# Performance work log

Hardware: AMD Instinct MI355X
Metric: run time of the kernel (lower is better)

## Reference

```python
import jax, jax.numpy as jnp
import numpy as np

WIN = 8   # window size
NH = 6    # num heads
DIM = 192
PDIM = 256
S = 32    # D=H=W spatial extent


def window_partition(x, w):
    # x: (B, D, H, W, C) -> (nW, w**3, C)
    B, D, H, Wd, C = x.shape
    x = x.reshape(B, D // w, w, H // w, w, Wd // w, w, C)
    x = x.transpose(0, 1, 3, 5, 2, 4, 6, 7)
    return x.reshape(-1, w * w * w, C)


def window_reverse(win, w, B, D, H, Wd):
    C = win.shape[-1]
    x = win.reshape(B, D // w, H // w, Wd // w, w, w, w, C)
    x = x.transpose(0, 1, 4, 2, 5, 3, 6, 7)
    return x.reshape(B, D, H, Wd, C)


def layernorm(x, g, b, eps=1e-5):
    m = x.mean(-1, keepdims=True)
    v = ((x - m) ** 2).mean(-1, keepdims=True)
    return (x - m) / jnp.sqrt(v + eps) * g + b


def setup_inputs() -> dict:
    key = jax.random.key(0)
    ks = jax.random.split(key, 8)
    return {
        "x": jax.random.normal(ks[0], (1, DIM, S, S, S), jnp.float32),
        "prev_x": jax.random.normal(ks[1], (1, PDIM, S, S, S), jnp.float32),
        "fc1_w": jax.random.normal(ks[2], (PDIM, PDIM), jnp.float32) * 0.02,
        "fc1_b": jnp.zeros((PDIM,), jnp.float32),
        "fc2_w": jax.random.normal(ks[3], (DIM, PDIM), jnp.float32) * 0.02,
        "fc2_b": jnp.zeros((DIM,), jnp.float32),
        "q_w": jax.random.normal(ks[4], (DIM, DIM), jnp.float32) * 0.02,
        "q_b": jnp.zeros((DIM,), jnp.float32),
        "kv_w": jax.random.normal(ks[5], (2 * DIM, DIM), jnp.float32) * 0.02,
        "v_b": jnp.zeros((DIM,), jnp.float32),
        "proj_w": jax.random.normal(ks[6], (DIM, DIM), jnp.float32) * 0.02,
        "proj_b": jnp.zeros((DIM,), jnp.float32),
        "logit_scale": jnp.log(10.0) * jnp.ones((NH, 1, 1), jnp.float32),
        "ln_g": jnp.ones((DIM,), jnp.float32),
        "ln_b": jnp.zeros((DIM,), jnp.float32),
    }


def reference(x, prev_x, fc1_w, fc1_b, fc2_w, fc2_b, q_w, q_b, kv_w, v_b,
              proj_w, proj_b, logit_scale, ln_g, ln_b):
    B, C, D, H, Wd = x.shape
    xc = x.transpose(0, 2, 3, 4, 1)       # (B, D, H, W, C)
    pc = prev_x.transpose(0, 2, 3, 4, 1)   # (B, D, H, W, prev_dim)
    # mlp_match: Linear -> GELU(exact) -> Linear
    pc = jax.nn.gelu(pc @ fc1_w.T + fc1_b, approximate=False) @ fc2_w.T + fc2_b
    xw = window_partition(xc, WIN)         # (nW, N, C)
    pw = window_partition(pc, WIN)         # (nW, N, C)
    nW, N, _ = xw.shape
    hd = C // NH
    # q from x1, kv from x2 (k has no bias, v does)
    q = (xw @ q_w.T + q_b).reshape(nW, N, NH, hd).transpose(0, 2, 1, 3)
    kv_bias = jnp.concatenate([jnp.zeros_like(v_b), v_b])
    kv = (pw @ kv_w.T + kv_bias).reshape(nW, N, 2, NH, hd).transpose(2, 0, 3, 1, 4)
    k_, v_ = kv[0], kv[1]                  # (nW, H, N, hd)
    # cosine attention with clamped learned logit scale
    qn = q / jnp.maximum(jnp.linalg.norm(q, axis=-1, keepdims=True), 1e-12)
    kn = k_ / jnp.maximum(jnp.linalg.norm(k_, axis=-1, keepdims=True), 1e-12)
    scale = jnp.exp(jnp.minimum(logit_scale, jnp.log(1.0 / 0.01)))  # (H,1,1)
    attn = jnp.einsum('whnd,whmd->whnm', qn, kn) * scale
    attn = jax.nn.softmax(attn, axis=-1)
    out = jnp.einsum('whnm,whmd->whnd', attn, v_).transpose(0, 2, 1, 3).reshape(nW, N, C)
    out = out @ proj_w.T + proj_b
    xw = xw + layernorm(out, ln_g, ln_b)   # residual + cross_norm
    xr = window_reverse(xw, WIN, B, D, H, Wd)
    return xr.transpose(0, 4, 1, 2, 3)     # back to (B, C, D, H, W)
```

## Files before the change

kernel.cpp:

```cpp
#include <hip/hip_runtime.h>
#include <stdint.h>

typedef unsigned short u16;
typedef unsigned int u32;
typedef short short8 __attribute__((ext_vector_type(8)));
typedef float f32x4 __attribute__((ext_vector_type(4)));
typedef u32 u32x4 __attribute__((ext_vector_type(4)));

#define T_TOT 32768

__device__ __forceinline__ u16 f2bf(float f) {
  u32 u = __float_as_uint(f);
  return (u16)((u + 0x7fffu + ((u >> 16) & 1u)) >> 16);
}
__device__ __forceinline__ float bf2f(u16 h) {
  return __uint_as_float(((u32)h) << 16);
}
__device__ __forceinline__ u32 pk2(float a, float b) {
  return (u32)f2bf(a) | ((u32)f2bf(b) << 16);
}
__device__ __forceinline__ u32 cvtpk(float a, float b) {
  u32 r;
  asm("v_cvt_pk_bf16_f32 %0, %1, %2" : "=v"(r) : "v"(a), "v"(b));
  return r;
}
__device__ __forceinline__ void unp8(uint4 d, float* v) {
  u32 dd[4] = {d.x, d.y, d.z, d.w};
#pragma unroll
  for (int q2 = 0; q2 < 4; ++q2) {
    v[q2 * 2]     = bf2f((u16)(dd[q2] & 0xffffu));
    v[q2 * 2 + 1] = bf2f((u16)(dd[q2] >> 16));
  }
}

__device__ __forceinline__ void gld_lds16(const void* g, void* l) {
  __builtin_amdgcn_global_load_lds(
      (const __attribute__((address_space(1))) u32*)g,
      (__attribute__((address_space(3))) u32*)l, 16, 0, 0);
}

__device__ __forceinline__ void plswap(u32& a, u32& b) {
#if __has_builtin(__builtin_amdgcn_permlane32_swap) && \
    __has_builtin(__builtin_amdgcn_permlane16_swap)
  typedef u32 u32x2v __attribute__((ext_vector_type(2)));
  u32x2v r = __builtin_amdgcn_permlane32_swap(a, b, false, false);
  u32x2v w = __builtin_amdgcn_permlane16_swap(r[0], r[1], false, false);
  a = w[0]; b = w[1];
#else
  asm volatile(
      "s_nop 2\n\t"
      "v_permlane32_swap_b32 %0, %1\n\t"
      "s_nop 2\n\t"
      "v_permlane16_swap_b32 %0, %1\n\t"
      "s_nop 2"
      : "+v"(a), "+v"(b));
#endif
}

__global__ __launch_bounds__(256) void k_wconv(
    const float* __restrict__ fc1, const float* __restrict__ fc2,
    const float* __restrict__ qw, const float* __restrict__ kvw,
    const float* __restrict__ pw, u16* __restrict__ out) {
  int idx = blockIdx.x * 256 + threadIdx.x;
  const float* src; int K; int rel; u16* dst;
  if (idx < 8192)       { src = fc1; K = 256; rel = idx;         dst = out; }
  else if (idx < 14336) { src = fc2; K = 256; rel = idx - 8192;  dst = out + 65536; }
  else if (idx < 18944) { src = qw;  K = 192; rel = idx - 14336; dst = out + 114688; }
  else if (idx < 28160) { src = kvw; K = 192; rel = idx - 18944; dst = out + 151552; }
  else                  { src = pw;  K = 192; rel = idx - 28160; dst = out + 225280; }
  int nch = K >> 3;
  int m = rel / nch, ch = rel % nch;
  const float* sp = src + (size_t)m * K + ch * 8;
  int pos = (ch & ~7) | ((ch ^ m) & 7);
  u16* dp = dst + (size_t)m * K + pos * 8;
  ushort4 u0, u1;
  u0.x = f2bf(sp[0]); u0.y = f2bf(sp[1]); u0.z = f2bf(sp[2]); u0.w = f2bf(sp[3]);
  u1.x = f2bf(sp[4]); u1.y = f2bf(sp[5]); u1.z = f2bf(sp[6]); u1.w = f2bf(sp[7]);
  *(ushort4*)(dp) = u0;
  *(ushort4*)(dp + 4) = u1;
}

template<int C>
__global__ __launch_bounds__(256) void k_transpose(const float* __restrict__ src,
                                                   u16* __restrict__ dst) {
  __shared__ u16 sT[64][72];
  int c0 = blockIdx.x * 64, t0 = blockIdx.y * 64;
  int tid = threadIdx.x;
  for (int i = tid; i < 1024; i += 256) {
    int row = i >> 4;
    int tb  = (i & 15) * 4;
    const float* sp = src + (size_t)(c0 + row) * T_TOT + t0 + tb;
    float4 v = *(const float4*)sp;
    ushort4 u;
    u.x = f2bf(v.x); u.y = f2bf(v.y); u.z = f2bf(v.z); u.w = f2bf(v.w);
    *(ushort4*)(&sT[row][tb]) = u;
  }
  __syncthreads();
  int tl = tid & 63;
  int jb = tid >> 6;
  for (int p = 0; p < 2; ++p) {
    int j = jb + 4 * p;
    int t = t0 + tl;
    u16 e[8];
#pragma unroll
    for (int e8 = 0; e8 < 8; ++e8) e[e8] = sT[j * 8 + e8][tl];
    int pos = (c0 >> 3) + (j ^ (t & 7));
    uint4 o;
    o.x = (u32)e[0] | ((u32)e[1] << 16);
    o.y = (u32)e[2] | ((u32)e[3] << 16);
    o.z = (u32)e[4] | ((u32)e[5] << 16);
    o.w = (u32)e[6] | ((u32)e[7] << 16);
    *(uint4*)(dst + (size_t)t * C + pos * 8) = o;
  }
}

enum { EPI_FC1 = 0, EPI_FC2 = 1, EPI_Q = 2, EPI_KV = 3 };

template<int M, int K, int EPI>
__global__ __launch_bounds__(256) void k_gemm(const u16* __restrict__ W,
    const u16* __restrict__ B, const float* __restrict__ bias,
    u16* __restrict__ out, u16* __restrict__ out2) {
  __shared__ u16 lW[64 * 64];
  __shared__ u16 lB[128 * 64];
  int tid = threadIdx.x;
  int lane = tid & 63, wid = tid >> 6;
  int g = lane >> 4, c = lane & 15;
  int wm = wid >> 1, wt = wid & 1;
  int t0 = blockIdx.x * 128, m0 = blockIdx.y * 64;
  f32x4 acc[2][4];
#pragma unroll
  for (int i = 0; i < 2; ++i)
#pragma unroll
    for (int j = 0; j < 4; ++j) acc[i][j] = f32x4{0.f, 0.f, 0.f, 0.f};

  for (int s = 0; s < K / 64; ++s) {
    __syncthreads();
#pragma unroll
    for (int i0 = 0; i0 < 512; i0 += 256) {
      int i = i0 + tid;
      int r = i >> 3, ch = i & 7;
      gld_lds16(W + (size_t)(m0 + r) * K + s * 64 + ch * 8,
                lW + (size_t)(i & ~63) * 8);
    }
#pragma unroll
    for (int i0 = 0; i0 < 1024; i0 += 256) {
      int i = i0 + tid;
      int r = i >> 3, ch = i & 7;
      gld_lds16(B + (size_t)(t0 + r) * K + s * 64 + ch * 8,
                lB + (size_t)(i & ~63) * 8);
    }
    __syncthreads();
#pragma unroll
    for (int kc = 0; kc < 2; ++kc) {
      short8 af[2], bfr[4];
#pragma unroll
      for (int mt = 0; mt < 2; ++mt) {
        int r = wm * 32 + mt * 16 + c;
        af[mt] = *(const short8*)(lW + r * 64 + (((kc * 4 + g) ^ (r & 7)) << 3));
      }
#pragma unroll
      for (int tt = 0; tt < 4; ++tt) {
        int r = wt * 64 + tt * 16 + c;
        bfr[tt] = *(const short8*)(lB + r * 64 + (((kc * 4 + g) ^ (r & 7)) << 3));
      }
#pragma unroll
      for (int mt = 0; mt < 2; ++mt)
#pragma unroll
        for (int tt = 0; tt < 4; ++tt)
          acc[mt][tt] = __builtin_amdgcn_mfma_f32_16x16x32_bf16(
              af[mt], bfr[tt], acc[mt][tt], 0, 0, 0);
    }
  }

#pragma unroll
  for (int mt = 0; mt < 2; ++mt) {
    int m_base = m0 + wm * 32 + mt * 16 + 4 * g;
    float br[4];
    if constexpr (EPI == EPI_KV) {
      if (m_base < 192) { br[0] = br[1] = br[2] = br[3] = 0.f; }
      else {
        float4 b4 = *(const float4*)(bias + (m_base - 192));
        br[0] = b4.x; br[1] = b4.y; br[2] = b4.z; br[3] = b4.w;
      }
    } else {
      float4 b4 = *(const float4*)(bias + m_base);
      br[0] = b4.x; br[1] = b4.y; br[2] = b4.z; br[3] = b4.w;
    }
#pragma unroll
    for (int tt = 0; tt < 4; ++tt) {
      int t = t0 + wt * 64 + tt * 16 + c;
      float v[4];
#pragma unroll
      for (int r = 0; r < 4; ++r) v[r] = acc[mt][tt][r] + br[r];
      if constexpr (EPI == EPI_FC1) {
#pragma unroll
        for (int r = 0; r < 4; ++r)
          v[r] = 0.5f * v[r] * (1.0f + erff(v[r] * 0.70710678118654752f));
      }
      if constexpr (EPI == EPI_FC1 || EPI == EPI_FC2) {
        ushort4 u;
        u.x = f2bf(v[0]); u.y = f2bf(v[1]); u.z = f2bf(v[2]); u.w = f2bf(v[3]);
        int pos = (m_base >> 3) ^ (t & 7);
        *(ushort4*)(out + (size_t)t * M + (pos << 3) + (m_base & 7)) = u;
      } else {
        int z = t >> 10, y = (t >> 5) & 31, xx = t & 31;
        int win = ((z >> 3) << 4) + ((y >> 3) << 2) + (xx >> 3);
        int n = ((z & 7) << 6) + ((y & 7) << 3) + (xx & 7);
        if (EPI == EPI_Q || m_base < 192) {
          int head = m_base >> 5, dim = m_base & 31;
          ushort4 u;
          u.x = f2bf(v[0]); u.y = f2bf(v[1]); u.z = f2bf(v[2]); u.w = f2bf(v[3]);
          *(ushort4*)(out + ((size_t)(win * 6 + head) * 512 + n) * 32 + dim) = u;
        } else {
          int vb = m_base - 192;
          int head = vb >> 5, dimb = vb & 31;
#pragma unroll
          for (int r = 0; r < 4; ++r) {
            int dimr = dimb + r;
            out2[((size_t)(win * 6 + head) * 32 + dimr) * 512 +
                 (((n >> 3) ^ (dimr & 7)) << 3) + (n & 7)] = f2bf(v[r]);
          }
        }
      }
    }
  }
}

__global__ __launch_bounds__(256) void k_attn(const u16* __restrict__ Qw,
    const u16* __restrict__ Kw, const u16* __restrict__ Vw,
    const float* __restrict__ ls, u16* __restrict__ Amat) {
  __shared__ u16 Kn[512 * 36];
  int tid = threadIdx.x, lane = tid & 63, wid = tid >> 6;
  int g = lane >> 4, c = lane & 15;
  int zq = blockIdx.x / 6, head = blockIdx.x % 6, win = blockIdx.y;
  const u16* Kg = Kw + (size_t)(win * 6 + head) * 16384;
  const u16* Vg = Vw + (size_t)(win * 6 + head) * 16384;
  const u16* Qg = Qw + (size_t)(win * 6 + head) * 16384;
  for (int i = tid; i < 2048; i += 256) {
    int r = i >> 2, ch = i & 3;
    *(uint4*)(Kn + r * 36 + ch * 8) = *(const uint4*)(Kg + (size_t)i * 8);
  }
  __syncthreads();

#pragma unroll
  for (int rep = 0; rep < 2; ++rep) {
    u16* kp = Kn + (rep * 256 + tid) * 36;
    float v[32];
    unp8(*(const uint4*)(kp), v);
    unp8(*(const uint4*)(kp + 8), v + 8);
    unp8(*(const uint4*)(kp + 16), v + 16);
    unp8(*(const uint4*)(kp + 24), v + 24);
    float ss = 0.f;
#pragma unroll
    for (int e = 0; e < 32; ++e) ss += v[e] * v[e];
    float rn = 1.0f / fmaxf(sqrtf(ss), 1e-12f);
#pragma unroll
    for (int i2 = 0; i2 < 4; ++i2) {
      uint4 d;
      d.x = pk2(v[i2 * 8 + 0] * rn, v[i2 * 8 + 1] * rn);
      d.y = pk2(v[i2 * 8 + 2] * rn, v[i2 * 8 + 3] * rn);
      d.z = pk2(v[i2 * 8 + 4] * rn, v[i2 * 8 + 5] * rn);
      d.w = pk2(v[i2 * 8 + 6] * rn, v[i2 * 8 + 7] * rn);
      *(uint4*)(kp + i2 * 8) = d;
    }
  }
  __syncthreads();

  float sl2e = __expf(fminf(ls[head], 4.6051701859880914f)) * 1.4426950408889634f;
  int wz = win >> 4, wy = (win >> 2) & 3, wx = win & 3;
  u32x4 onepk;
  onepk[0] = 0x3F803F80u; onepk[1] = 0x3F803F80u;
  onepk[2] = 0x3F803F80u; onepk[3] = 0x3F803F80u;
  short8 ONES = __builtin_bit_cast(short8, onepk);

  for (int qp = 0; qp < 2; ++qp) {
    int q0A = zq * 256 + wid * 64 + qp * 32;
    int q0B = q0A + 16;
    uint4 qrA = *(const uint4*)(Qg + (size_t)(q0A + c) * 32 + g * 8);
    uint4 qrB = *(const uint4*)(Qg + (size_t)(q0B + c) * 32 + g * 8);
    float qvA[8], qvB[8];
    unp8(qrA, qvA);
    unp8(qrB, qvB);
    float ssA = 0.f, ssB = 0.f;
#pragma unroll
    for (int e = 0; e < 8; ++e) { ssA += qvA[e] * qvA[e]; ssB += qvB[e] * qvB[e]; }
    ssA += __shfl_xor(ssA, 16); ssA += __shfl_xor(ssA, 32);
    ssB += __shfl_xor(ssB, 16); ssB += __shfl_xor(ssB, 32);
    float rnA = sl2e / fmaxf(sqrtf(ssA), 1e-12f);
    float rnB = sl2e / fmaxf(sqrtf(ssB), 1e-12f);
    u32x4 qpkA, qpkB;
#pragma unroll
    for (int e = 0; e < 4; ++e) {
      qpkA[e] = pk2(qvA[e * 2] * rnA, qvA[e * 2 + 1] * rnA);
      qpkB[e] = pk2(qvB[e * 2] * rnB, qvB[e * 2 + 1] * rnB);
    }
    short8 qfA = __builtin_bit_cast(short8, qpkA);
    short8 qfB = __builtin_bit_cast(short8, qpkB);

    f32x4 o0A = {0.f, 0.f, 0.f, 0.f}, o1A = {0.f, 0.f, 0.f, 0.f};
    f32x4 o2A = {0.f, 0.f, 0.f, 0.f};
    f32x4 o0B = {0.f, 0.f, 0.f, 0.f}, o1B = {0.f, 0.f, 0.f, 0.f};
    f32x4 o2B = {0.f, 0.f, 0.f, 0.f};
#pragma unroll 2
    for (int cc = 0; cc < 16; ++cc) {
      short8 kf0 = *(const short8*)(Kn + (size_t)(cc * 32 + c) * 36 + g * 8);
      short8 kf1 = *(const short8*)(Kn + (size_t)(cc * 32 + 16 + c) * 36 + g * 8);
      int chpos = ((cc * 4 + g) ^ (c & 7)) << 3;
      short8 vf0 = *(const short8*)(Vg + (size_t)c * 512 + chpos);
      short8 vf1 = *(const short8*)(Vg + (size_t)(16 + c) * 512 + chpos);
      f32x4 s0A = __builtin_amdgcn_mfma_f32_16x16x32_bf16(
          kf0, qfA, f32x4{0.f, 0.f, 0.f, 0.f}, 0, 0, 0);
      f32x4 s1A = __builtin_amdgcn_mfma_f32_16x16x32_bf16(
          kf1, qfA, f32x4{0.f, 0.f, 0.f, 0.f}, 0, 0, 0);
      f32x4 s0B = __builtin_amdgcn_mfma_f32_16x16x32_bf16(
          kf0, qfB, f32x4{0.f, 0.f, 0.f, 0.f}, 0, 0, 0);
      f32x4 s1B = __builtin_amdgcn_mfma_f32_16x16x32_bf16(
          kf1, qfB, f32x4{0.f, 0.f, 0.f, 0.f}, 0, 0, 0);
      f32x4 p0A, p1A, p0B, p1B;
#pragma unroll
      for (int r = 0; r < 4; ++r) {
        p0A[r] = __builtin_amdgcn_exp2f(s0A[r]);
        p1A[r] = __builtin_amdgcn_exp2f(s1A[r]);
        p0B[r] = __builtin_amdgcn_exp2f(s0B[r]);
        p1B[r] = __builtin_amdgcn_exp2f(s1B[r]);
      }
      u32 waA = cvtpk(p0A[0], p0A[1]), wbA = cvtpk(p0A[2], p0A[3]);
      u32 wcA = cvtpk(p1A[0], p1A[1]), wdA = cvtpk(p1A[2], p1A[3]);
      plswap(waA, wcA);
      plswap(wbA, wdA);
      u32 waB = cvtpk(p0B[0], p0B[1]), wbB = cvtpk(p0B[2], p0B[3]);
      u32 wcB = cvtpk(p1B[0], p1B[1]), wdB = cvtpk(p1B[2], p1B[3]);
      plswap(waB, wcB);
      plswap(wbB, wdB);
      u32x4 pwA, pwB;
      pwA[0] = waA; pwA[1] = wbA; pwA[2] = wcA; pwA[3] = wdA;
      pwB[0] = waB; pwB[1] = wbB; pwB[2] = wcB; pwB[3] = wdB;
      short8 pfA = __builtin_bit_cast(short8, pwA);
      short8 pfB = __builtin_bit_cast(short8, pwB);
      o0A = __builtin_amdgcn_mfma_f32_16x16x32_bf16(pfA, vf0, o0A, 0, 0, 0);
      o1A = __builtin_amdgcn_mfma_f32_16x16x32_bf16(pfA, vf1, o1A, 0, 0, 0);
      o2A = __builtin_amdgcn_mfma_f32_16x16x32_bf16(pfA, ONES, o2A, 0, 0, 0);
      o0B = __builtin_amdgcn_mfma_f32_16x16x32_bf16(pfB, vf0, o0B, 0, 0, 0);
      o1B = __builtin_amdgcn_mfma_f32_16x16x32_bf16(pfB, vf1, o1B, 0, 0, 0);
      o2B = __builtin_amdgcn_mfma_f32_16x16x32_bf16(pfB, ONES, o2B, 0, 0, 0);
    }

#pragma unroll
    for (int half = 0; half < 2; ++half) {
      f32x4 oo0 = half ? o0B : o0A;
      f32x4 oo1 = half ? o1B : o1A;
      f32x4 osum = half ? o2B : o2A;
      int q0 = half ? q0B : q0A;
      int cg0 = head * 32 + c;
      int cg1 = cg0 + 16;
#pragma unroll
      for (int r = 0; r < 4; ++r) {
        float rs = 1.0f / osum[r];
        int n = q0 + 4 * g + r;
        int dz = n >> 6, dy = (n >> 3) & 7, dx = n & 7;
        int t = (wz * 8 + dz) * 1024 + (wy * 8 + dy) * 32 + wx * 8 + dx;
        Amat[(size_t)t * 192 + (((cg0 >> 3) ^ (t & 7)) << 3) + (cg0 & 7)] =
            f2bf(oo0[r] * rs);
        Amat[(size_t)t * 192 + (((cg1 >> 3) ^ (t & 7)) << 3) + (cg1 & 7)] =
            f2bf(oo1[r] * rs);
      }
    }
  }
}

__global__ __launch_bounds__(256) void k_proj_ln(const u16* __restrict__ W,
    const u16* __restrict__ B, const float* __restrict__ bias,
    const float* __restrict__ x, const float* __restrict__ gg,
    const float* __restrict__ bb, float* __restrict__ out) {
  __shared__ u16 lW[192 * 64];
  __shared__ u16 lB[64 * 64];
  __shared__ float red[2][4][64];
  int tid = threadIdx.x;
  int lane = tid & 63, wid = tid >> 6;
  int g = lane >> 4, c = lane & 15;
  int t0 = blockIdx.x * 64;
  f32x4 acc[3][4];
#pragma unroll
  for (int i = 0; i < 3; ++i)
#pragma unroll
    for (int j = 0; j < 4; ++j) acc[i][j] = f32x4{0.f, 0.f, 0.f, 0.f};

  for (int s = 0; s < 3; ++s) {
    __syncthreads();
#pragma unroll
    for (int i0 = 0; i0 < 1536; i0 += 256) {
      int i = i0 + tid;
      int r = i >> 3, ch = i & 7;
      gld_lds16(W + (size_t)r * 192 + s * 64 + ch * 8,
                lW + (size_t)(i & ~63) * 8);
    }
    {
      int i = tid + (tid >= 0 ? 0 : 0);
#pragma unroll
      for (int i0 = 0; i0 < 512; i0 += 256) {
        int ii = i0 + tid;
        int r = ii >> 3, ch = ii & 7;
        gld_lds16(B + (size_t)(t0 + r) * 192 + s * 64 + ch * 8,
                  lB + (size_t)(ii & ~63) * 8);
      }
      (void)i;
    }
    __syncthreads();
#pragma unroll
    for (int kc = 0; kc < 2; ++kc) {
      short8 af[3], bfr[4];
#pragma unroll
      for (int mt = 0; mt < 3; ++mt) {
        int r = wid * 48 + mt * 16 + c;
        af[mt] = *(const short8*)(lW + r * 64 + (((kc * 4 + g) ^ (r & 7)) << 3));
      }
#pragma unroll
      for (int tt = 0; tt < 4; ++tt) {
        int r = tt * 16 + c;
        bfr[tt] = *(const short8*)(lB + r * 64 + (((kc * 4 + g) ^ (r & 7)) << 3));
      }
#pragma unroll
      for (int mt = 0; mt < 3; ++mt)
#pragma unroll
        for (int tt = 0; tt < 4; ++tt)
          acc[mt][tt] = __builtin_amdgcn_mfma_f32_16x16x32_bf16(
              af[mt], bfr[tt], acc[mt][tt], 0, 0, 0);
    }
  }

  float br[3][4];
#pragma unroll
  for (int mt = 0; mt < 3; ++mt) {
    float4 b4 = *(const float4*)(bias + wid * 48 + mt * 16 + 4 * g);
    br[mt][0] = b4.x; br[mt][1] = b4.y; br[mt][2] = b4.z; br[mt][3] = b4.w;
  }
  float s1[4], s2[4];
#pragma unroll
  for (int tt = 0; tt < 4; ++tt) {
    s1[tt] = 0.f; s2[tt] = 0.f;
#pragma unroll
    for (int mt = 0; mt < 3; ++mt)
#pragma unroll
      for (int r = 0; r < 4; ++r) {
        float v = acc[mt][tt][r] + br[mt][r];
        s1[tt] += v;
        s2[tt] += v * v;
      }
    s1[tt] += __shfl_xor(s1[tt], 16); s1[tt] += __shfl_xor(s1[tt], 32);
    s2[tt] += __shfl_xor(s2[tt], 16); s2[tt] += __shfl_xor(s2[tt], 32);
  }
  if (lane < 16) {
#pragma unroll
    for (int tt = 0; tt < 4; ++tt) {
      red[0][wid][tt * 16 + lane] = s1[tt];
      red[1][wid][tt * 16 + lane] = s2[tt];
    }
  }
  __syncthreads();
  float mean[4], rstd[4];
#pragma unroll
  for (int tt = 0; tt < 4; ++tt) {
    int tl = tt * 16 + c;
    float S1 = (red[0][0][tl] + red[0][1][tl]) + (red[0][2][tl] + red[0][3][tl]);
    float S2 = (red[1][0][tl] + red[1][1][tl]) + (red[1][2][tl] + red[1][3][tl]);
    float m = S1 * (1.0f / 192.0f);
    float var = S2 * (1.0f / 192.0f) - m * m;
    mean[tt] = m;
    rstd[tt] = rsqrtf(var + 1e-5f);
  }
#pragma unroll
  for (int mt = 0; mt < 3; ++mt) {
    int m_base = wid * 48 + mt * 16 + 4 * g;
#pragma unroll
    for (int r = 0; r < 4; ++r) {
      int ch = m_base + r;
      float ga = gg[ch], ba = bb[ch];
      const float* xp = x + (size_t)ch * T_TOT + t0;
      float* op = out + (size_t)ch * T_TOT + t0;
#pragma unroll
      for (int tt = 0; tt < 4; ++tt) {
        int tl = tt * 16 + c;
        float v = acc[mt][tt][r] + br[mt][r];
        op[tl] = xp[tl] + (v - mean[tt]) * rstd[tt] * ga + ba;
      }
    }
  }
}

extern "C" void kernel_launch(void* const* d_in, const int* in_sizes, int n_in,
                              void* d_out, int out_size, void* d_ws, size_t ws_size,
                              hipStream_t stream) {
  const float* x      = (const float*)d_in[0];
  const float* prev   = (const float*)d_in[1];
  const float* fc1_w  = (const float*)d_in[2];
  const float* fc1_b  = (const float*)d_in[3];
  const float* fc2_w  = (const float*)d_in[4];
  const float* fc2_b  = (const float*)d_in[5];
  const float* q_w    = (const float*)d_in[6];
  const float* q_b    = (const float*)d_in[7];
  const float* kv_w   = (const float*)d_in[8];
  const float* v_b    = (const float*)d_in[9];
  const float* proj_w = (const float*)d_in[10];
  const float* proj_b = (const float*)d_in[11];
  const float* lsc    = (const float*)d_in[12];
  const float* ln_g   = (const float*)d_in[13];
  const float* ln_b   = (const float*)d_in[14];
  float* out = (float*)d_out;
  char* ws = (char*)d_ws;

  u16* Pt   = (u16*)(ws + 0);
  u16* Y1t  = (u16*)(ws + 16777216);
  u16* Zt   = (u16*)(ws + 33554432);
  u16* Xt   = (u16*)(ws + 46137344);
  u16* Kwin = (u16*)(ws + 58720256);
  u16* Vwin = (u16*)(ws + 71303168);
  u16* Wbf  = (u16*)(ws + 83886080);
  u16* Qwin = Pt;
  u16* Amat = Y1t;

  k_wconv<<<128, 256, 0, stream>>>(fc1_w, fc2_w, q_w, kv_w, proj_w, Wbf);
  k_transpose<256><<<dim3(4, 512), 256, 0, stream>>>(prev, Pt);
  k_transpose<192><<<dim3(3, 512), 256, 0, stream>>>(x, Xt);
  k_gemm<256, 256, EPI_FC1><<<dim3(256, 4), 256, 0, stream>>>(Wbf, Pt, fc1_b, Y1t, nullptr);
  k_gemm<192, 256, EPI_FC2><<<dim3(256, 3), 256, 0, stream>>>(Wbf + 65536, Y1t, fc2_b, Zt, nullptr);
  k_gemm<192, 192, EPI_Q><<<dim3(256, 3), 256, 0, stream>>>(Wbf + 114688, Xt, q_b, Qwin, nullptr);
  k_gemm<384, 192, EPI_KV><<<dim3(256, 6), 256, 0, stream>>>(Wbf + 151552, Zt, v_b, Kwin, Vwin);
  k_attn<<<dim3(12, 64), 256, 0, stream>>>(Qwin, Kwin, Vwin, lsc, Amat);
  k_proj_ln<<<512, 256, 0, stream>>>(Wbf + 225280, Amat, proj_b, x, ln_g, ln_b, out);
}
```

Before: 128.2 us.

## Fuse Q/K normalization and logit scale into projection GEMM epilogues

Moves the per-head L2 normalization of Q (with the clamped exp logit scale folded in) and of K into the epilogues of the Q and KV projection GEMMs. It uses cross-lane shuffles over the 32-dim head slice. K is written pre-padded to a 36-element row stride so the attention kernel can load it straight into LDS with global_load_lds, with no normalize pass and one fewer barrier. Q fragments are read directly as MFMA operands. The cost is extra epilogue work in the GEMMs, a larger K buffer, and a changed workspace layout in which Kwin now overlaps Xt.

Result: faster. 125.1 us (-2.5%).

```diff
diff --git a/kernel.cpp b/kernel.cpp
--- a/kernel.cpp
+++ b/kernel.cpp
@@ -23,14 +23,6 @@
   u32 r;
   asm("v_cvt_pk_bf16_f32 %0, %1, %2" : "=v"(r) : "v"(a), "v"(b));
   return r;
-}
-__device__ __forceinline__ void unp8(uint4 d, float* v) {
-  u32 dd[4] = {d.x, d.y, d.z, d.w};
-#pragma unroll
-  for (int q2 = 0; q2 < 4; ++q2) {
-    v[q2 * 2]     = bf2f((u16)(dd[q2] & 0xffffu));
-    v[q2 * 2 + 1] = bf2f((u16)(dd[q2] >> 16));
-  }
 }
 
 __device__ __forceinline__ void gld_lds16(const void* g, void* l) {
@@ -119,6 +111,7 @@
 template<int M, int K, int EPI>
 __global__ __launch_bounds__(256) void k_gemm(const u16* __restrict__ W,
     const u16* __restrict__ B, const float* __restrict__ bias,
+    const float* __restrict__ ls,
     u16* __restrict__ out, u16* __restrict__ out2) {
   __shared__ u16 lW[64 * 64];
   __shared__ u16 lB[128 * 64];
@@ -172,6 +165,7 @@
     }
   }
 
+  float vv[2][4][4];
 #pragma unroll
   for (int mt = 0; mt < 2; ++mt) {
     int m_base = m0 + wm * 32 + mt * 16 + 4 * g;
@@ -187,11 +181,45 @@
       br[0] = b4.x; br[1] = b4.y; br[2] = b4.z; br[3] = b4.w;
     }
 #pragma unroll
+    for (int tt = 0; tt < 4; ++tt)
+#pragma unroll
+      for (int r = 0; r < 4; ++r) vv[mt][tt][r] = acc[mt][tt][r] + br[r];
+  }
+
+  if constexpr (EPI == EPI_Q || EPI == EPI_KV) {
+    if (EPI == EPI_Q || m0 < 192) {
+      float sc = 1.0f;
+      if constexpr (EPI == EPI_Q) {
+        int headq = (m0 + wm * 32) >> 5;
+        sc = __expf(fminf(ls[headq], 4.6051701859880914f)) * 1.4426950408889634f;
+      }
+#pragma unroll
+      for (int tt = 0; tt < 4; ++tt) {
+        float ss = 0.f;
+#pragma unroll
+        for (int mt = 0; mt < 2; ++mt)
+#pragma unroll
+          for (int r = 0; r < 4; ++r) ss += vv[mt][tt][r] * vv[mt][tt][r];
+        ss += __shfl_xor(ss, 16);
+        ss += __shfl_xor(ss, 32);
+        float rn = sc / fmaxf(sqrtf(ss), 1e-12f);
+#pragma unroll
+        for (int mt = 0; mt < 2; ++mt)
+#pragma unroll
+          for (int r = 0; r < 4; ++r) vv[mt][tt][r] *= rn;
+      }
+    }
+  }
+
+#pragma unroll
+  for (int mt = 0; mt < 2; ++mt) {
+    int m_base = m0 + wm * 32 + mt * 16 + 4 * g;
+#pragma unroll
     for (int tt = 0; tt < 4; ++tt) {
       int t = t0 + wt * 64 + tt * 16 + c;
       float v[4];
 #pragma unroll
-      for (int r = 0; r < 4; ++r) v[r] = acc[mt][tt][r] + br[r];
+      for (int r = 0; r < 4; ++r) v[r] = vv[mt][tt][r];
       if constexpr (EPI == EPI_FC1) {
 #pragma unroll
         for (int r = 0; r < 4; ++r)
@@ -206,11 +234,16 @@
         int z = t >> 10, y = (t >> 5) & 31, xx = t & 31;
         int win = ((z >> 3) << 4) + ((y >> 3) << 2) + (xx >> 3);
         int n = ((z & 7) << 6) + ((y & 7) << 3) + (xx & 7);
-        if (EPI == EPI_Q || m_base < 192) {
+        if (EPI == EPI_Q) {
           int head = m_base >> 5, dim = m_base & 31;
           ushort4 u;
           u.x = f2bf(v[0]); u.y = f2bf(v[1]); u.z = f2bf(v[2]); u.w = f2bf(v[3]);
           *(ushort4*)(out + ((size_t)(win * 6 + head) * 512 + n) * 32 + dim) = u;
+        } else if (m_base < 192) {
+          int head = m_base >> 5, dim = m_base & 31;
+          ushort4 u;
+          u.x = f2bf(v[0]); u.y = f2bf(v[1]); u.z = f2bf(v[2]); u.w = f2bf(v[3]);
+          *(ushort4*)(out + ((size_t)(win * 6 + head) * 512 + n) * 36 + dim) = u;
         } else {
           int vb = m_base - 192;
           int head = vb >> 5, dimb = vb & 31;
@@ -228,45 +261,18 @@
 
 __global__ __launch_bounds__(256) void k_attn(const u16* __restrict__ Qw,
     const u16* __restrict__ Kw, const u16* __restrict__ Vw,
-    const float* __restrict__ ls, u16* __restrict__ Amat) {
+    u16* __restrict__ Amat) {
   __shared__ u16 Kn[512 * 36];
   int tid = threadIdx.x, lane = tid & 63, wid = tid >> 6;
   int g = lane >> 4, c = lane & 15;
   int zq = blockIdx.x / 6, head = blockIdx.x % 6, win = blockIdx.y;
-  const u16* Kg = Kw + (size_t)(win * 6 + head) * 16384;
+  const u16* Kg = Kw + (size_t)(win * 6 + head) * 18432;
   const u16* Vg = Vw + (size_t)(win * 6 + head) * 16384;
   const u16* Qg = Qw + (size_t)(win * 6 + head) * 16384;
-  for (int i = tid; i < 2048; i += 256) {
-    int r = i >> 2, ch = i & 3;
-    *(uint4*)(Kn + r * 36 + ch * 8) = *(const uint4*)(Kg + (size_t)i * 8);
-  }
+  for (int i = tid; i < 2304; i += 256)
+    gld_lds16(Kg + (size_t)i * 8, Kn + (size_t)i * 8);
   __syncthreads();
 
-#pragma unroll
-  for (int rep = 0; rep < 2; ++rep) {
-    u16* kp = Kn + (rep * 256 + tid) * 36;
-    float v[32];
-    unp8(*(const uint4*)(kp), v);
-    unp8(*(const uint4*)(kp + 8), v + 8);
-    unp8(*(const uint4*)(kp + 16), v + 16);
-    unp8(*(const uint4*)(kp + 24), v + 24);
-    float ss = 0.f;
-#pragma unroll
-    for (int e = 0; e < 32; ++e) ss += v[e] * v[e];
-    float rn = 1.0f / fmaxf(sqrtf(ss), 1e-12f);
-#pragma unroll
-    for (int i2 = 0; i2 < 4; ++i2) {
-      uint4 d;
-      d.x = pk2(v[i2 * 8 + 0] * rn, v[i2 * 8 + 1] * rn);
-      d.y = pk2(v[i2 * 8 + 2] * rn, v[i2 * 8 + 3] * rn);
-      d.z = pk2(v[i2 * 8 + 4] * rn, v[i2 * 8 + 5] * rn);
-      d.w = pk2(v[i2 * 8 + 6] * rn, v[i2 * 8 + 7] * rn);
-      *(uint4*)(kp + i2 * 8) = d;
-    }
-  }
-  __syncthreads();
-
-  float sl2e = __expf(fminf(ls[head], 4.6051701859880914f)) * 1.4426950408889634f;
   int wz = win >> 4, wy = (win >> 2) & 3, wx = win & 3;
   u32x4 onepk;
   onepk[0] = 0x3F803F80u; onepk[1] = 0x3F803F80u;
@@ -276,26 +282,8 @@
   for (int qp = 0; qp < 2; ++qp) {
     int q0A = zq * 256 + wid * 64 + qp * 32;
     int q0B = q0A + 16;
-    uint4 qrA = *(const uint4*)(Qg + (size_t)(q0A + c) * 32 + g * 8);
-    uint4 qrB = *(const uint4*)(Qg + (size_t)(q0B + c) * 32 + g * 8);
-    float qvA[8], qvB[8];
-    unp8(qrA, qvA);
-    unp8(qrB, qvB);
-    float ssA = 0.f, ssB = 0.f;
-#pragma unroll
-    for (int e = 0; e < 8; ++e) { ssA += qvA[e] * qvA[e]; ssB += qvB[e] * qvB[e]; }
-    ssA += __shfl_xor(ssA, 16); ssA += __shfl_xor(ssA, 32);
-    ssB += __shfl_xor(ssB, 16); ssB += __shfl_xor(ssB, 32);
-    float rnA = sl2e / fmaxf(sqrtf(ssA), 1e-12f);
-    float rnB = sl2e / fmaxf(sqrtf(ssB), 1e-12f);
-    u32x4 qpkA, qpkB;
-#pragma unroll
-    for (int e = 0; e < 4; ++e) {
-      qpkA[e] = pk2(qvA[e * 2] * rnA, qvA[e * 2 + 1] * rnA);
-      qpkB[e] = pk2(qvB[e * 2] * rnB, qvB[e * 2 + 1] * rnB);
-    }
-    short8 qfA = __builtin_bit_cast(short8, qpkA);
-    short8 qfB = __builtin_bit_cast(short8, qpkB);
+    short8 qfA = *(const short8*)(Qg + (size_t)(q0A + c) * 32 + g * 8);
+    short8 qfB = *(const short8*)(Qg + (size_t)(q0B + c) * 32 + g * 8);
 
     f32x4 o0A = {0.f, 0.f, 0.f, 0.f}, o1A = {0.f, 0.f, 0.f, 0.f};
     f32x4 o2A = {0.f, 0.f, 0.f, 0.f};
@@ -394,16 +382,12 @@
       gld_lds16(W + (size_t)r * 192 + s * 64 + ch * 8,
                 lW + (size_t)(i & ~63) * 8);
     }
-    {
-      int i = tid + (tid >= 0 ? 0 : 0);
-#pragma unroll
-      for (int i0 = 0; i0 < 512; i0 += 256) {
-        int ii = i0 + tid;
-        int r = ii >> 3, ch = ii & 7;
-        gld_lds16(B + (size_t)(t0 + r) * 192 + s * 64 + ch * 8,
-                  lB + (size_t)(ii & ~63) * 8);
-      }
-      (void)i;
+#pragma unroll
+    for (int i0 = 0; i0 < 512; i0 += 256) {
+      int ii = i0 + tid;
+      int r = ii >> 3, ch = ii & 7;
+      gld_lds16(B + (size_t)(t0 + r) * 192 + s * 64 + ch * 8,
+                lB + (size_t)(ii & ~63) * 8);
     }
     __syncthreads();
 #pragma unroll
@@ -512,19 +496,19 @@
   u16* Y1t  = (u16*)(ws + 16777216);
   u16* Zt   = (u16*)(ws + 33554432);
   u16* Xt   = (u16*)(ws + 46137344);
-  u16* Kwin = (u16*)(ws + 58720256);
-  u16* Vwin = (u16*)(ws + 71303168);
-  u16* Wbf  = (u16*)(ws + 83886080);
+  u16* Kwin = (u16*)(ws + 46137344);
+  u16* Vwin = (u16*)(ws + 60293120);
+  u16* Wbf  = (u16*)(ws + 72876032);
   u16* Qwin = Pt;
   u16* Amat = Y1t;
 
   k_wconv<<<128, 256, 0, stream>>>(fc1_w, fc2_w, q_w, kv_w, proj_w, Wbf);
   k_transpose<256><<<dim3(4, 512), 256, 0, stream>>>(prev, Pt);
   k_transpose<192><<<dim3(3, 512), 256, 0, stream>>>(x, Xt);
-  k_gemm<256, 256, EPI_FC1><<<dim3(256, 4), 256, 0, stream>>>(Wbf, Pt, fc1_b, Y1t, nullptr);
-  k_gemm<192, 256, EPI_FC2><<<dim3(256, 3), 256, 0, stream>>>(Wbf + 65536, Y1t, fc2_b, Zt, nullptr);
-  k_gemm<192, 192, EPI_Q><<<dim3(256, 3), 256, 0, stream>>>(Wbf + 114688, Xt, q_b, Qwin, nullptr);
-  k_gemm<384, 192, EPI_KV><<<dim3(256, 6), 256, 0, stream>>>(Wbf + 151552, Zt, v_b, Kwin, Vwin);
-  k_attn<<<dim3(12, 64), 256, 0, stream>>>(Qwin, Kwin, Vwin, lsc, Amat);
+  k_gemm<256, 256, EPI_FC1><<<dim3(256, 4), 256, 0, stream>>>(Wbf, Pt, fc1_b, nullptr, Y1t, nullptr);
+  k_gemm<192, 256, EPI_FC2><<<dim3(256, 3), 256, 0, stream>>>(Wbf + 65536, Y1t, fc2_b, nullptr, Zt, nullptr);
+  k_gemm<192, 192, EPI_Q><<<dim3(256, 3), 256, 0, stream>>>(Wbf + 114688, Xt, q_b, lsc, Qwin, nullptr);
+  k_gemm<384, 192, EPI_KV><<<dim3(256, 6), 256, 0, stream>>>(Wbf + 151552, Zt, v_b, nullptr, Kwin, Vwin);
+  k_attn<<<dim3(12, 64), 256, 0, stream>>>(Qwin, Kwin, Vwin, Amat);
   k_proj_ln<<<512, 256, 0, stream>>>(Wbf + 225280, Amat, proj_b, x, ln_g, ln_b, out);
 }
```
